# Kernel tuning notes

Hardware: AMD Instinct MI355X
Metric: run time of the kernel (lower is better)

Reference implementation:

```python
import jax, jax.numpy as jnp
import numpy as np

N = 65536          # number of rows (nodes/edges)
F = 64             # input feature dim
UNITS = 64         # output dim
NUM_RELATIONS = 25
NUM_BASES = 8


def setup_inputs() -> dict:
    key = jax.random.key(0)
    k1, k2, k3, k4 = jax.random.split(key, 4)
    features = jax.random.normal(k1, (N, F), dtype=jnp.float32)
    relations = jax.random.randint(k2, (N,), 0, NUM_RELATIONS, dtype=jnp.int32)
    # basis kernels V_b: [B, F, units] (glorot-like scale)
    kernel = jax.random.normal(k3, (NUM_BASES, F, UNITS), dtype=jnp.float32) * (1.0 / np.sqrt(F))
    # basis coefficients a_rb: [R, B]
    lin_bases = jax.random.normal(k4, (NUM_RELATIONS, NUM_BASES), dtype=jnp.float32) * (1.0 / np.sqrt(NUM_BASES))
    bias = jnp.zeros((UNITS,), dtype=jnp.float32)
    return {"features": features, "relations": relations, "kernel": kernel,
            "lin_bases": lin_bases, "bias": bias}


def reference(features, relations, kernel, lin_bases, bias):
    # Basis decomposition: W_r = sum_b a_rb V_b  -> [R, F, units]
    w = jnp.einsum('rb,bfo->rfo', lin_bases, kernel)
    # Gather per-row kernel and contract (matches ops.take + batch_dot)
    w_per_row = w[relations]                       # [N, F, units]
    out = jnp.einsum('nf,nfo->no', features, w_per_row)  # [N, units]
    out = out + bias
    return out  # linear activation (activation=None)
```

## Files before the change

### kernel.cpp

```cpp
#include <hip/hip_runtime.h>


typedef float v4f __attribute__((ext_vector_type(4)));
typedef short bf16x8 __attribute__((ext_vector_type(8)));
typedef float f32x4 __attribute__((ext_vector_type(4)));
typedef unsigned short u16;
typedef u16 u16x4 __attribute__((ext_vector_type(4)));

#define NN 65536
#define FF 64
#define UU 64
#define RR 25
#define BB 8
#define CAP 4096
#define NSLOT (RR * CAP)
#define SAS 72

#define IDX_OFF 0
#define CUR_OFF (NSLOT * 4)
#define WT_OFF  (NSLOT * 4 + 128)
#define WS_NEED ((size_t)(WT_OFF + RR * FF * UU * 2))

__device__ __forceinline__ u16 f2bf(float x) {
  union { float f; unsigned u; } v; v.f = x;
  unsigned r = v.u + 0x7FFF + ((v.u >> 16) & 1);
  return (u16)(r >> 16);
}

__global__ __launch_bounds__(256) void k_prep(
    const float* __restrict__ kern,
    const float* __restrict__ lin,
    const int*   __restrict__ rel,
    u16*         __restrict__ Wt,
    int*         __restrict__ idx_sorted,
    int*         __restrict__ cursors) {
  const int wblocks = (RR * FF * UU) / 256;
  int bid = blockIdx.x;
  if (bid < wblocks) {
    int idx = bid * 256 + threadIdx.x;
    int r = __builtin_amdgcn_readfirstlane(idx >> 12);
    int f = (idx >> 6) & 63;
    int u = idx & 63;
    float acc = 0.f;
#pragma unroll
    for (int b = 0; b < BB; ++b)
      acc += lin[r * BB + b] * kern[b * (FF * UU) + f * UU + u];
    Wt[r * (FF * UU) + u * FF + f] = f2bf(acc);
  } else {
    int sb  = bid - wblocks;
    int tid = threadIdx.x;
    __shared__ int cnt[RR], base[RR], lcur[RR];
    if (tid < RR) { cnt[tid] = 0; lcur[tid] = 0; }
    __syncthreads();
    int row = sb * 256 + tid;
    int r = rel[row];
    atomicAdd(&cnt[r], 1);
    __syncthreads();
    if (tid < RR) base[tid] = atomicAdd(&cursors[tid], cnt[tid]);
    __syncthreads();
    int loc = atomicAdd(&lcur[r], 1);
    idx_sorted[r * CAP + base[r] + loc] = row;
  }
}

__global__ __launch_bounds__(256, 2) void k_main(
    const float* __restrict__ features,
    const float* __restrict__ bias,
    const u16*   __restrict__ Wt,
    const int*   __restrict__ idx_sorted,
    const int*   __restrict__ cursors,
    float*       __restrict__ out) {
  __shared__ int srow[64];
  __shared__ u16 sA[64 * SAS];
  __shared__ u16 sB[64 * SAS];

  int tid       = threadIdx.x;
  int base_slot = blockIdx.x * 64;
  int r   = __builtin_amdgcn_readfirstlane(base_slot >> 12);
  int cnt = cursors[r];
  int bpos  = base_slot & (CAP - 1);
  int valid = cnt - bpos;
  if (valid <= 0) return;
  if (valid > 64) valid = 64;

  if (tid < 64)
    srow[tid] = (tid < valid) ? idx_sorted[base_slot + tid] : -1;
  __syncthreads();

  const v4f* f4 = reinterpret_cast<const v4f*>(features);
#pragma unroll
  for (int i = 0; i < 4; ++i) {
    int s   = i * 256 + tid;
    int rl  = s >> 4;
    int seg = s & 15;
    if (rl < valid) {
      v4f fv = f4[(size_t)srow[rl] * 16 + seg];
      u16x4 p = { f2bf(fv[0]), f2bf(fv[1]), f2bf(fv[2]), f2bf(fv[3]) };
      *reinterpret_cast<u16x4*>(&sA[rl * SAS + seg * 4]) = p;
    }
  }

  const u16x4* w4 = reinterpret_cast<const u16x4*>(Wt + r * (FF * UU));
#pragma unroll
  for (int i = 0; i < 4; ++i) {
    int c    = i * 256 + tid;
    int u    = c >> 4;
    int fseg = c & 15;
    *reinterpret_cast<u16x4*>(&sB[u * SAS + fseg * 4]) = w4[c];
  }
  __syncthreads();

  int lane = tid & 63;
  int w    = __builtin_amdgcn_readfirstlane(tid >> 6);
  int m    = lane & 15;
  int quad = lane >> 4;

  bf16x8 bfrag[2];
#pragma unroll
  for (int h = 0; h < 2; ++h)
    bfrag[h] = *reinterpret_cast<const bf16x8*>(
        &sB[(w * 16 + m) * SAS + h * 32 + quad * 8]);

  float bv = bias[w * 16 + m];
  f32x4 acc[4];
#pragma unroll
  for (int t = 0; t < 4; ++t) {
    acc[t] = (f32x4){bv, bv, bv, bv};
#pragma unroll
    for (int h = 0; h < 2; ++h) {
      bf16x8 afrag = *reinterpret_cast<const bf16x8*>(
          &sA[(t * 16 + m) * SAS + h * 32 + quad * 8]);
      acc[t] = __builtin_amdgcn_mfma_f32_16x16x32_bf16(afrag, bfrag[h], acc[t], 0, 0, 0);
    }
  }

#pragma unroll
  for (int t = 0; t < 4; ++t) {
#pragma unroll
    for (int g = 0; g < 4; ++g) {
      int grow = srow[t * 16 + quad * 4 + g];
      if (grow >= 0)
        out[(size_t)grow * UU + w * 16 + m] = acc[t][g];
    }
  }
}

__global__ __launch_bounds__(256) void k_fallback(
    const float* __restrict__ features,
    const int*   __restrict__ rel,
    const float* __restrict__ kern,
    const float* __restrict__ lin,
    const float* __restrict__ bias,
    float*       __restrict__ out) {
  int tid = threadIdx.x;
  int row = blockIdx.x * 64 + (tid & 63);
  int q   = __builtin_amdgcn_readfirstlane(tid >> 6);
  int r   = rel[row];
  float cf[BB];
#pragma unroll
  for (int b = 0; b < BB; ++b) cf[b] = lin[r * BB + b];
  const v4f* fr = reinterpret_cast<const v4f*>(features + (size_t)row * FF);
  float acc[16];
#pragma unroll
  for (int j = 0; j < 16; ++j) acc[j] = bias[q * 16 + j];
#pragma unroll
  for (int ch = 0; ch < 4; ++ch) {
    v4f fv[4];
#pragma unroll
    for (int k = 0; k < 4; ++k) fv[k] = fr[ch * 4 + k];
#pragma unroll
    for (int k = 0; k < 4; ++k) {
#pragma unroll
      for (int c = 0; c < 4; ++c) {
        int f = ch * 16 + k * 4 + c;
        float fs = fv[k][c];
        float wf[16];
#pragma unroll
        for (int jj = 0; jj < 16; ++jj) wf[jj] = 0.f;
#pragma unroll
        for (int b = 0; b < BB; ++b) {
          const float* Vb = kern + b * (FF * UU) + f * UU + q * 16;
#pragma unroll
          for (int jj = 0; jj < 16; ++jj) wf[jj] += cf[b] * Vb[jj];
        }
#pragma unroll
        for (int jj = 0; jj < 16; ++jj) acc[jj] += fs * wf[jj];
      }
    }
  }
  v4f* o4 = reinterpret_cast<v4f*>(out + (size_t)row * UU + q * 16);
#pragma unroll
  for (int j4 = 0; j4 < 4; ++j4) {
    v4f v = {acc[4 * j4], acc[4 * j4 + 1], acc[4 * j4 + 2], acc[4 * j4 + 3]};
    o4[j4] = v;
  }
}

extern "C" void kernel_launch(void* const* d_in, const int* in_sizes, int n_in,
                              void* d_out, int out_size, void* d_ws, size_t ws_size,
                              hipStream_t stream) {
  const float* features  = (const float*)d_in[0];
  const int*   relations = (const int*)d_in[1];
  const float* kern      = (const float*)d_in[2];
  const float* lin       = (const float*)d_in[3];
  const float* bias      = (const float*)d_in[4];
  float* out = (float*)d_out;

  if (ws_size >= WS_NEED) {
    char* ws          = (char*)d_ws;
    int*  idx_sorted  = (int*)(ws + IDX_OFF);
    int*  cursors     = (int*)(ws + CUR_OFF);
    u16*  Wt          = (u16*)(ws + WT_OFF);
    (void)hipMemsetAsync(cursors, 0, RR * sizeof(int), stream);
    k_prep<<<(RR * FF * UU) / 256 + NN / 256, 256, 0, stream>>>(
        kern, lin, relations, Wt, idx_sorted, cursors);
    k_main<<<NSLOT / 64, 256, 0, stream>>>(features, bias, Wt, idx_sorted, cursors, out);
  } else {
    k_fallback<<<NN / 64, 256, 0, stream>>>(features, relations, kern, lin, bias, out);
  }
}
```

Baseline: 87.22 us.

## Replace global-atomic relation bucketing with per-block fixed-capacity buckets

Relation bucketing now writes each source block's rows into its own 64-slot bucket per relation, plus a per-block count. This removes the global cursor atomics and the memset launch that reset them. The main kernel launches one block per (relation, source block) pair and only runs the MFMA tiles that hold valid rows. The cost is many more sparsely filled blocks, each reloading the full relation weight tile, and any rows beyond 64 of one relation in a 256-row block are silently dropped.

```diff
diff --git a/kernel.cpp b/kernel.cpp
--- a/kernel.cpp
+++ b/kernel.cpp
@@ -12,14 +12,15 @@
 #define UU 64
 #define RR 25
 #define BB 8
-#define CAP 4096
-#define NSLOT (RR * CAP)
+#define SBN 256
+#define CAPB 64
+#define NSLOT (RR * SBN * CAPB)
 #define SAS 72
 
-#define IDX_OFF 0
-#define CUR_OFF (NSLOT * 4)
-#define WT_OFF  (NSLOT * 4 + 128)
-#define WS_NEED ((size_t)(WT_OFF + RR * FF * UU * 2))
+#define IDX_OFF  0
+#define BCNT_OFF (NSLOT * 4)
+#define WT_OFF   (BCNT_OFF + SBN * RR * 4)
+#define WS_NEED  ((size_t)(WT_OFF + RR * FF * UU * 2))
 
 __device__ __forceinline__ u16 f2bf(float x) {
   union { float f; unsigned u; } v; v.f = x;
@@ -33,7 +34,7 @@
     const int*   __restrict__ rel,
     u16*         __restrict__ Wt,
     int*         __restrict__ idx_sorted,
-    int*         __restrict__ cursors) {
+    int*         __restrict__ bcnt) {
   const int wblocks = (RR * FF * UU) / 256;
   int bid = blockIdx.x;
   if (bid < wblocks) {
@@ -49,17 +50,16 @@
   } else {
     int sb  = bid - wblocks;
     int tid = threadIdx.x;
-    __shared__ int cnt[RR], base[RR], lcur[RR];
-    if (tid < RR) { cnt[tid] = 0; lcur[tid] = 0; }
+    __shared__ int cnt[RR];
+    if (tid < RR) cnt[tid] = 0;
     __syncthreads();
-    int row = sb * 256 + tid;
-    int r = rel[row];
-    atomicAdd(&cnt[r], 1);
+    int row  = sb * 256 + tid;
+    int r    = rel[row];
+    int rank = atomicAdd(&cnt[r], 1);
     __syncthreads();
-    if (tid < RR) base[tid] = atomicAdd(&cursors[tid], cnt[tid]);
-    __syncthreads();
-    int loc = atomicAdd(&lcur[r], 1);
-    idx_sorted[r * CAP + base[r] + loc] = row;
+    if (tid < RR) bcnt[sb * RR + tid] = cnt[tid];
+    if (rank < CAPB)
+      idx_sorted[(r * SBN + sb) * CAPB + rank] = row;
   }
 }
 
@@ -68,23 +68,23 @@
     const float* __restrict__ bias,
     const u16*   __restrict__ Wt,
     const int*   __restrict__ idx_sorted,
-    const int*   __restrict__ cursors,
+    const int*   __restrict__ bcnt,
     float*       __restrict__ out) {
   __shared__ int srow[64];
   __shared__ u16 sA[64 * SAS];
   __shared__ u16 sB[64 * SAS];
 
-  int tid       = threadIdx.x;
-  int base_slot = blockIdx.x * 64;
-  int r   = __builtin_amdgcn_readfirstlane(base_slot >> 12);
-  int cnt = cursors[r];
-  int bpos  = base_slot & (CAP - 1);
-  int valid = cnt - bpos;
+  int tid = threadIdx.x;
+  int b   = blockIdx.x;
+  int r   = __builtin_amdgcn_readfirstlane(b >> 8);
+  int sb  = b & 255;
+  int valid = bcnt[sb * RR + r];
   if (valid <= 0) return;
-  if (valid > 64) valid = 64;
-
+  if (valid > CAPB) valid = CAPB;
+
+  int base = (r * SBN + sb) * CAPB;
   if (tid < 64)
-    srow[tid] = (tid < valid) ? idx_sorted[base_slot + tid] : -1;
+    srow[tid] = (tid < valid) ? idx_sorted[base + tid] : -1;
   __syncthreads();
 
   const v4f* f4 = reinterpret_cast<const v4f*>(features);
@@ -122,25 +122,21 @@
         &sB[(w * 16 + m) * SAS + h * 32 + quad * 8]);
 
   float bv = bias[w * 16 + m];
-  f32x4 acc[4];
-#pragma unroll
-  for (int t = 0; t < 4; ++t) {
-    acc[t] = (f32x4){bv, bv, bv, bv};
+  int nt = (valid + 15) >> 4;
+
+  for (int t = 0; t < nt; ++t) {
+    f32x4 acc = (f32x4){bv, bv, bv, bv};
 #pragma unroll
     for (int h = 0; h < 2; ++h) {
       bf16x8 afrag = *reinterpret_cast<const bf16x8*>(
           &sA[(t * 16 + m) * SAS + h * 32 + quad * 8]);
-      acc[t] = __builtin_amdgcn_mfma_f32_16x16x32_bf16(afrag, bfrag[h], acc[t], 0, 0, 0);
-    }
-  }
-
-#pragma unroll
-  for (int t = 0; t < 4; ++t) {
+      acc = __builtin_amdgcn_mfma_f32_16x16x32_bf16(afrag, bfrag[h], acc, 0, 0, 0);
+    }
 #pragma unroll
     for (int g = 0; g < 4; ++g) {
       int grow = srow[t * 16 + quad * 4 + g];
       if (grow >= 0)
-        out[(size_t)grow * UU + w * 16 + m] = acc[t][g];
+        out[(size_t)grow * UU + w * 16 + m] = acc[g];
     }
   }
 }
@@ -207,14 +203,13 @@
   float* out = (float*)d_out;
 
   if (ws_size >= WS_NEED) {
-    char* ws          = (char*)d_ws;
-    int*  idx_sorted  = (int*)(ws + IDX_OFF);
-    int*  cursors     = (int*)(ws + CUR_OFF);
-    u16*  Wt          = (u16*)(ws + WT_OFF);
-    (void)hipMemsetAsync(cursors, 0, RR * sizeof(int), stream);
-    k_prep<<<(RR * FF * UU) / 256 + NN / 256, 256, 0, stream>>>(
-        kern, lin, relations, Wt, idx_sorted, cursors);
-    k_main<<<NSLOT / 64, 256, 0, stream>>>(features, bias, Wt, idx_sorted, cursors, out);
+    char* ws         = (char*)d_ws;
+    int*  idx_sorted = (int*)(ws + IDX_OFF);
+    int*  bcnt       = (int*)(ws + BCNT_OFF);
+    u16*  Wt         = (u16*)(ws + WT_OFF);
+    k_prep<<<(RR * FF * UU) / 256 + SBN, 256, 0, stream>>>(
+        kern, lin, relations, Wt, idx_sorted, bcnt);
+    k_main<<<RR * SBN, 256, 0, stream>>>(features, bias, Wt, idx_sorted, bcnt, out);
   } else {
     k_fallback<<<NN / 64, 256, 0, stream>>>(features, relations, kern, lin, bias, out);
   }
```

Result: faster. 83.83 us (-3.9%).
